# Kernel optimization log

Hardware: AMD Instinct MI355X
Metric: run time of the kernel (lower is better)

## Reference

```python
import jax, jax.numpy as jnp
import numpy as np

B, T, H, M = 8, 2048, 1024, 256


def setup_inputs() -> dict:
    key = jax.random.key(0)
    ks = jax.random.split(key, 8)
    hidden_states = jax.random.normal(ks[0], (B, T, H), jnp.float32)
    incoming_signal = jax.random.normal(ks[1], (B, T, H), jnp.float32)
    top_down = jax.random.normal(ks[2], (B, T, H), jnp.float32)
    basis = jax.random.normal(ks[3], (B, H, M), jnp.float32) / np.float32(np.sqrt(H))
    # coupling L = G^-1; near identity for a near-orthonormal basis
    coupling = jnp.tile(jnp.eye(M, dtype=jnp.float32), (B, 1, 1)) + 0.01 * jax.random.normal(ks[4], (B, M, M), jnp.float32)
    W_rec = jax.random.normal(ks[5], (2 * M, H), jnp.float32) / np.float32(np.sqrt(2 * M))
    tape0_re = 0.1 * jax.random.normal(ks[6], (B, M), jnp.float32)
    tape0_im = 0.1 * jax.random.normal(ks[7], (B, M), jnp.float32)
    # raw metaparams: sigmoid(gamma_raw)=0.9, softplus(beta_raw)=0.05 (init values in source)
    gamma_raw = jnp.float32(np.log(0.9 / 0.1))
    beta_raw = jnp.float32(np.log(np.expm1(0.05)))
    return dict(hidden_states=hidden_states, incoming_signal=incoming_signal, top_down=top_down,
                basis=basis, coupling=coupling, W_rec=W_rec, tape0_re=tape0_re, tape0_im=tape0_im,
                bottom_up_gain=jnp.float32(1.0), top_down_gain=jnp.float32(1.0), self_rec_gain=jnp.float32(1.0),
                gamma_raw=gamma_raw, beta_raw=beta_raw)


def reference(hidden_states, incoming_signal, top_down, basis, coupling, W_rec,
              tape0_re, tape0_im, bottom_up_gain, top_down_gain, self_rec_gain,
              gamma_raw, beta_raw):
    gamma = jax.nn.sigmoid(gamma_raw)      # transient decay
    beta = jax.nn.softplus(beta_raw)       # binding scale
    # gated combination of external + bottom-up + top-down signals
    combined = hidden_states + bottom_up_gain * incoming_signal + top_down_gain * top_down  # [B,T,H]
    # delayed self-recurrence: project real/imag tape features back into hidden space
    tape_feat = jnp.concatenate([tape0_re, tape0_im], axis=-1)          # [B,2M]
    combined = combined + self_rec_gain * (tape_feat @ W_rec)[:, None, :]
    # coupled reception (vectorized over tokens): w = E^T v ; alpha = L w
    w = jnp.einsum('btd,bdm->btm', combined, basis)                     # [B,T,M]
    alpha = jnp.einsum('btm,bmn->btn', w, coupling)                     # [B,T,M]
    # recurrent tape update (binding write + transient decay), c = alpha * s
    def step(carry, a_t):
        s_re, s_im = carry
        s_re = gamma * s_re + beta * a_t
        s_im = gamma * s_im
        return (s_re, s_im), a_t * s_re
    (_, _), c_re = jax.lax.scan(step, (tape0_re, tape0_im), jnp.swapaxes(alpha, 0, 1))
    c_re = jnp.swapaxes(c_re, 0, 1)                                     # [B,T,M]
    # readout through the basis
    y = jnp.einsum('btm,bdm->btd', c_re, basis)                         # [B,T,H]
    return y
```

## Files before the change

### kernel.cpp

```cpp
#include <hip/hip_runtime.h>
#include <hip/hip_bf16.h>

#define B_  8
#define T_  2048
#define H_  1024
#define M_  256

typedef __bf16 bf16x8 __attribute__((ext_vector_type(8)));
typedef float  f32x4  __attribute__((ext_vector_type(4)));
typedef unsigned short us4 __attribute__((ext_vector_type(4)));
typedef unsigned short us8 __attribute__((ext_vector_type(8)));

__device__ inline unsigned short f2bf(float f) {
    unsigned int u = __builtin_bit_cast(unsigned int, f);
    return (unsigned short)((u + 0x7FFFu + ((u >> 16) & 1u)) >> 16);
}
__device__ inline float bf2f(unsigned short u) {
    unsigned int x = ((unsigned int)u) << 16;
    return __builtin_bit_cast(float, x);
}

__global__ void k_bias(const float* __restrict__ W, const float* __restrict__ re,
                       const float* __restrict__ im, const float* __restrict__ g_srg,
                       float* __restrict__ bias)
{
    int b = blockIdx.x;
    int h0 = blockIdx.y * 64;
    int lane = threadIdx.x & 63, w = threadIdx.x >> 6;
    int h = h0 + lane;
    float acc = 0.f;
    #pragma unroll 4
    for (int m = w * 64; m < w * 64 + 64; ++m) {
        float rv = re[b * M_ + m], iv = im[b * M_ + m];
        acc += rv * W[(size_t)m * H_ + h] + iv * W[(size_t)(M_ + m) * H_ + h];
    }
    __shared__ float sh[4][64];
    sh[w][lane] = acc;
    __syncthreads();
    if (w == 0)
        bias[b * H_ + h] = g_srg[0] * (sh[0][lane] + sh[1][lane] + sh[2][lane] + sh[3][lane]);
}

__global__ void k_cast(const float* __restrict__ basis, unsigned short* __restrict__ basisB)
{
    size_t i = ((size_t)blockIdx.x * 256 + threadIdx.x) * 8;
    float4 a = *(const float4*)&basis[i];
    float4 b = *(const float4*)&basis[i + 4];
    us8 o = { f2bf(a.x), f2bf(a.y), f2bf(a.z), f2bf(a.w),
              f2bf(b.x), f2bf(b.y), f2bf(b.z), f2bf(b.w) };
    *(us8*)&basisB[i] = o;
}

__global__ void k_cplT(const float* __restrict__ cpl, unsigned short* __restrict__ cplT)
{
    int b = blockIdx.z, r0 = blockIdx.x * 64, c0 = blockIdx.y * 64;
    __shared__ float t[64][65];
    int tid = threadIdx.x;
    #pragma unroll
    for (int i = 0; i < 4; ++i) {
        int u = tid + i * 256;
        int r = u >> 4, c4 = (u & 15) * 4;
        float4 v = *(const float4*)&cpl[((size_t)(b * M_ + r0 + r)) * M_ + c0 + c4];
        t[r][c4] = v.x; t[r][c4 + 1] = v.y; t[r][c4 + 2] = v.z; t[r][c4 + 3] = v.w;
    }
    __syncthreads();
    #pragma unroll
    for (int i = 0; i < 4; ++i) {
        int u = tid + i * 256;
        int m = u >> 4, r4 = (u & 15) * 4;
        us4 o = { f2bf(t[r4][m]), f2bf(t[r4 + 1][m]), f2bf(t[r4 + 2][m]), f2bf(t[r4 + 3][m]) };
        *(us4*)&cplT[((size_t)(b * M_ + c0 + m)) * M_ + r0 + r4] = o;
    }
}

__global__ __launch_bounds__(256) void k_b2(const unsigned short* __restrict__ cplT,
                                            const unsigned short* __restrict__ basisB,
                                            unsigned short* __restrict__ b2T)
{
    const int b = blockIdx.z;
    const int n0 = blockIdx.x * 64;
    const int h0 = blockIdx.y * 128;
    const int tid = threadIdx.x;
    const int lane = tid & 63, w = tid >> 6;

    __shared__ __align__(16) unsigned short As[64][72];
    __shared__ __align__(16) unsigned short Bs[128][72];

    const unsigned short* Ab = cplT + (size_t)(b * M_ + n0) * M_;
    const unsigned short* Bb = basisB + (size_t)(b * H_ + h0) * M_;

    f32x4 acc[4][2];
    #pragma unroll
    for (int i = 0; i < 4; ++i) { acc[i][0] = (f32x4){0,0,0,0}; acc[i][1] = (f32x4){0,0,0,0}; }

    const int rsel = lane & 15;
    const int kgrp = (lane >> 4) * 8;

    for (int k0 = 0; k0 < M_; k0 += 64) {
        #pragma unroll
        for (int i = 0; i < 2; ++i) {
            int u = tid + i * 256;
            int r = u >> 3, c8 = (u & 7) * 8;
            *(us8*)&As[r][c8] = *(const us8*)&Ab[(size_t)r * M_ + k0 + c8];
        }
        #pragma unroll
        for (int i = 0; i < 4; ++i) {
            int u = tid + i * 256;
            int r = u >> 3, c8 = (u & 7) * 8;
            *(us8*)&Bs[r][c8] = *(const us8*)&Bb[(size_t)r * M_ + k0 + c8];
        }
        __syncthreads();
        #pragma unroll
        for (int kk = 0; kk < 2; ++kk) {
            const int kb = kk * 32 + kgrp;
            bf16x8 af[4], bfr[2];
            #pragma unroll
            for (int mi = 0; mi < 4; ++mi) af[mi] = *(const bf16x8*)&As[mi * 16 + rsel][kb];
            #pragma unroll
            for (int ni = 0; ni < 2; ++ni) bfr[ni] = *(const bf16x8*)&Bs[w * 32 + ni * 16 + rsel][kb];
            #pragma unroll
            for (int mi = 0; mi < 4; ++mi)
                #pragma unroll
                for (int ni = 0; ni < 2; ++ni)
                    acc[mi][ni] = __builtin_amdgcn_mfma_f32_16x16x32_bf16(af[mi], bfr[ni], acc[mi][ni], 0, 0, 0);
        }
        __syncthreads();
    }

    unsigned short* ob = b2T + (size_t)(b * M_ + n0) * H_ + h0;
    const int rbase = (lane >> 4) * 4;
    #pragma unroll
    for (int mi = 0; mi < 4; ++mi)
        #pragma unroll
        for (int ni = 0; ni < 2; ++ni)
            #pragma unroll
            for (int r = 0; r < 4; ++r)
                ob[(size_t)(mi * 16 + rbase + r) * H_ + w * 32 + ni * 16 + rsel] = f2bf(acc[mi][ni][r]);
}

__global__ __launch_bounds__(1024) void k_alpha(
    const float* __restrict__ hs, const float* __restrict__ inc, const float* __restrict__ tdn,
    const unsigned short* __restrict__ b2T, const float* __restrict__ bias,
    const float* __restrict__ g_bu, const float* __restrict__ g_td,
    unsigned short* __restrict__ alpha16)
{
    const int b = blockIdx.y;
    const int t0 = blockIdx.x * 64;
    const int tid = threadIdx.x;
    const int lane = tid & 63, w = tid >> 6;
    const float bug = g_bu[0], tdg = g_td[0];

    __shared__ __align__(16) unsigned short As[64][72];
    __shared__ __align__(16) unsigned short Bs[256][72];

    const float* hsb = hs  + (size_t)(b * T_ + t0) * H_;
    const float* inb = inc + (size_t)(b * T_ + t0) * H_;
    const float* tdb = tdn + (size_t)(b * T_ + t0) * H_;
    const float* bib = bias + (size_t)b * H_;
    const unsigned short* Bb = b2T + (size_t)b * M_ * H_;

    f32x4 acc[4];
    #pragma unroll
    for (int i = 0; i < 4; ++i) acc[i] = (f32x4){0.f, 0.f, 0.f, 0.f};

    const int rsel = lane & 15;
    const int kgrp = (lane >> 4) * 8;

    for (int k0 = 0; k0 < H_; k0 += 64) {
        {
            int r = tid >> 4, c4 = (tid & 15) * 4;
            size_t g = (size_t)r * H_ + k0 + c4;
            float4 a = *(const float4*)(hsb + g);
            float4 e = *(const float4*)(inb + g);
            float4 d = *(const float4*)(tdb + g);
            float4 bi = *(const float4*)(bib + k0 + c4);
            us4 o = { f2bf(a.x + bug * e.x + tdg * d.x + bi.x),
                      f2bf(a.y + bug * e.y + tdg * d.y + bi.y),
                      f2bf(a.z + bug * e.z + tdg * d.z + bi.z),
                      f2bf(a.w + bug * e.w + tdg * d.w + bi.w) };
            *(us4*)&As[r][c4] = o;
        }
        #pragma unroll
        for (int i = 0; i < 2; ++i) {
            int u = tid + i * 1024;
            int m = u >> 3, c8 = (u & 7) * 8;
            *(us8*)&Bs[m][c8] = *(const us8*)&Bb[(size_t)m * H_ + k0 + c8];
        }
        __syncthreads();
        #pragma unroll
        for (int kk = 0; kk < 2; ++kk) {
            const int kb = kk * 32 + kgrp;
            bf16x8 af[4], bfr;
            #pragma unroll
            for (int mi = 0; mi < 4; ++mi) af[mi] = *(const bf16x8*)&As[mi * 16 + rsel][kb];
            bfr = *(const bf16x8*)&Bs[w * 16 + rsel][kb];
            #pragma unroll
            for (int mi = 0; mi < 4; ++mi)
                acc[mi] = __builtin_amdgcn_mfma_f32_16x16x32_bf16(af[mi], bfr, acc[mi], 0, 0, 0);
        }
        __syncthreads();
    }

    unsigned short* ab = alpha16 + (size_t)(b * T_ + t0) * M_;
    const int rbase = (lane >> 4) * 4;
    #pragma unroll
    for (int mi = 0; mi < 4; ++mi)
        #pragma unroll
        for (int r = 0; r < 4; ++r)
            ab[(size_t)(mi * 16 + rbase + r) * M_ + w * 16 + rsel] = f2bf(acc[mi][r]);
}

__global__ void k_scan(const unsigned short* __restrict__ alpha16, const float* __restrict__ tape_re,
                       const float* __restrict__ g_gr, const float* __restrict__ g_br,
                       unsigned short* __restrict__ cbuf)
{
    int b = blockIdx.y, chunk = blockIdx.x;
    int m = threadIdx.x;
    float graw = g_gr[0], braw = g_br[0];
    float gamma = 1.f / (1.f + __expf(-graw));
    float beta  = log1pf(__expf(braw));
    int t0 = chunk * 64;
    int th = (t0 >= 96) ? (t0 - 96) : 0;
    float s = tape_re[b * M_ + m];
    if (th > 0) s *= __powf(gamma, (float)th);
    const unsigned short* ab = alpha16 + (size_t)b * T_ * M_ + m;
    unsigned short* cb = cbuf + (size_t)b * T_ * M_ + m;
    for (int t = th; t < t0 + 64; ++t) {
        float a = bf2f(ab[(size_t)t * M_]);
        s = gamma * s + beta * a;
        if (t >= t0) cb[(size_t)t * M_] = f2bf(a * s);
    }
}

__global__ __launch_bounds__(256) void k_y(const unsigned short* __restrict__ cbuf,
                                           const unsigned short* __restrict__ basisB,
                                           float* __restrict__ out)
{
    const int b = blockIdx.z;
    const int t0 = blockIdx.x * 128;
    const int h0 = blockIdx.y * 128;
    const int tid = threadIdx.x;
    const int lane = tid & 63, w = tid >> 6;
    const int wm = w >> 1, wn = w & 1;

    __shared__ __align__(16) unsigned short As[128][72];
    __shared__ __align__(16) unsigned short Bs[128][72];

    const unsigned short* cb = cbuf + (size_t)(b * T_ + t0) * M_;
    const unsigned short* bb = basisB + (size_t)(b * H_ + h0) * M_;

    f32x4 acc[4][4];
    #pragma unroll
    for (int i = 0; i < 4; ++i)
        #pragma unroll
        for (int j = 0; j < 4; ++j)
            acc[i][j] = (f32x4){0.f, 0.f, 0.f, 0.f};

    const int rsel = lane & 15;
    const int kgrp = (lane >> 4) * 8;

    for (int k0 = 0; k0 < M_; k0 += 64) {
        #pragma unroll
        for (int i = 0; i < 4; ++i) {
            int u = tid + i * 256;
            int r = u >> 3, c8 = (u & 7) * 8;
            *(us8*)&As[r][c8] = *(const us8*)&cb[(size_t)r * M_ + k0 + c8];
        }
        #pragma unroll
        for (int i = 0; i < 4; ++i) {
            int u = tid + i * 256;
            int r = u >> 3, c8 = (u & 7) * 8;
            *(us8*)&Bs[r][c8] = *(const us8*)&bb[(size_t)r * M_ + k0 + c8];
        }
        __syncthreads();
        #pragma unroll
        for (int kk = 0; kk < 2; ++kk) {
            const int kb = kk * 32 + kgrp;
            bf16x8 af[4], bfr[4];
            #pragma unroll
            for (int mi = 0; mi < 4; ++mi) af[mi] = *(const bf16x8*)&As[wm * 64 + mi * 16 + rsel][kb];
            #pragma unroll
            for (int ni = 0; ni < 4; ++ni) bfr[ni] = *(const bf16x8*)&Bs[wn * 64 + ni * 16 + rsel][kb];
            #pragma unroll
            for (int mi = 0; mi < 4; ++mi)
                #pragma unroll
                for (int ni = 0; ni < 4; ++ni)
                    acc[mi][ni] = __builtin_amdgcn_mfma_f32_16x16x32_bf16(af[mi], bfr[ni], acc[mi][ni], 0, 0, 0);
        }
        __syncthreads();
    }

    float* ob = out + (size_t)(b * T_ + t0) * H_ + h0;
    const int rbase = (lane >> 4) * 4;
    #pragma unroll
    for (int mi = 0; mi < 4; ++mi)
        #pragma unroll
        for (int ni = 0; ni < 4; ++ni)
            #pragma unroll
            for (int r = 0; r < 4; ++r)
                ob[(size_t)(wm * 64 + mi * 16 + rbase + r) * H_ + wn * 64 + ni * 16 + rsel] = acc[mi][ni][r];
}

extern "C" void kernel_launch(void* const* d_in, const int* in_sizes, int n_in,
                              void* d_out, int out_size, void* d_ws, size_t ws_size,
                              hipStream_t stream)
{
    const float* hs   = (const float*)d_in[0];
    const float* inc  = (const float*)d_in[1];
    const float* tdn  = (const float*)d_in[2];
    const float* basis= (const float*)d_in[3];
    const float* cpl  = (const float*)d_in[4];
    const float* W    = (const float*)d_in[5];
    const float* t_re = (const float*)d_in[6];
    const float* t_im = (const float*)d_in[7];
    const float* g_bu = (const float*)d_in[8];
    const float* g_td = (const float*)d_in[9];
    const float* g_sr = (const float*)d_in[10];
    const float* g_gr = (const float*)d_in[11];
    const float* g_br = (const float*)d_in[12];
    float* out = (float*)d_out;

    char* ws = (char*)d_ws;
    float*          bias   = (float*)(ws);
    unsigned short* basisB = (unsigned short*)(ws + (1u << 16));
    unsigned short* cplT   = (unsigned short*)(ws + (1u << 16) + (4u << 20));
    unsigned short* b2T    = (unsigned short*)(ws + (1u << 16) + (5u << 20));
    unsigned short* alpha16= (unsigned short*)(ws + (1u << 16) + (9u << 20));
    unsigned short* cbuf   = (unsigned short*)(ws + (1u << 16) + (17u << 20));

    k_bias <<<dim3(B_, H_ / 64),            dim3(256),  0, stream>>>(W, t_re, t_im, g_sr, bias);
    k_cast <<<dim3((B_ * H_ * M_) / (256*8)), dim3(256), 0, stream>>>(basis, basisB);
    k_cplT <<<dim3(M_ / 64, M_ / 64, B_),   dim3(256),  0, stream>>>(cpl, cplT);
    k_b2   <<<dim3(M_ / 64, H_ / 128, B_),  dim3(256),  0, stream>>>(cplT, basisB, b2T);
    k_alpha<<<dim3(T_ / 64, B_),            dim3(1024), 0, stream>>>(hs, inc, tdn, b2T, bias, g_bu, g_td, alpha16);
    k_scan <<<dim3(T_ / 64, B_),            dim3(256),  0, stream>>>(alpha16, t_re, g_gr, g_br, cbuf);
    k_y    <<<dim3(T_ / 128, H_ / 128, B_), dim3(256),  0, stream>>>(cbuf, basisB, out);
}
```

Measured before the change: 152.6 us.

## Merge prep kernels and register-prefetch the alpha GEMM with smaller tiles

Result: faster. 149.5 us (-2.0%).

```diff
diff --git a/kernel.cpp b/kernel.cpp
--- a/kernel.cpp
+++ b/kernel.cpp
@@ -20,56 +20,57 @@
     return __builtin_bit_cast(float, x);
 }
 
-__global__ void k_bias(const float* __restrict__ W, const float* __restrict__ re,
+__global__ void k_prep(const float* __restrict__ basis, const float* __restrict__ cpl,
+                       const float* __restrict__ W, const float* __restrict__ re,
                        const float* __restrict__ im, const float* __restrict__ g_srg,
+                       unsigned short* __restrict__ basisB, unsigned short* __restrict__ cplT,
                        float* __restrict__ bias)
 {
-    int b = blockIdx.x;
-    int h0 = blockIdx.y * 64;
-    int lane = threadIdx.x & 63, w = threadIdx.x >> 6;
-    int h = h0 + lane;
-    float acc = 0.f;
-    #pragma unroll 4
-    for (int m = w * 64; m < w * 64 + 64; ++m) {
-        float rv = re[b * M_ + m], iv = im[b * M_ + m];
-        acc += rv * W[(size_t)m * H_ + h] + iv * W[(size_t)(M_ + m) * H_ + h];
-    }
-    __shared__ float sh[4][64];
-    sh[w][lane] = acc;
-    __syncthreads();
-    if (w == 0)
-        bias[b * H_ + h] = g_srg[0] * (sh[0][lane] + sh[1][lane] + sh[2][lane] + sh[3][lane]);
-}
-
-__global__ void k_cast(const float* __restrict__ basis, unsigned short* __restrict__ basisB)
-{
-    size_t i = ((size_t)blockIdx.x * 256 + threadIdx.x) * 8;
-    float4 a = *(const float4*)&basis[i];
-    float4 b = *(const float4*)&basis[i + 4];
-    us8 o = { f2bf(a.x), f2bf(a.y), f2bf(a.z), f2bf(a.w),
-              f2bf(b.x), f2bf(b.y), f2bf(b.z), f2bf(b.w) };
-    *(us8*)&basisB[i] = o;
-}
-
-__global__ void k_cplT(const float* __restrict__ cpl, unsigned short* __restrict__ cplT)
-{
-    int b = blockIdx.z, r0 = blockIdx.x * 64, c0 = blockIdx.y * 64;
-    __shared__ float t[64][65];
+    int blk = blockIdx.x;
     int tid = threadIdx.x;
-    #pragma unroll
-    for (int i = 0; i < 4; ++i) {
-        int u = tid + i * 256;
-        int r = u >> 4, c4 = (u & 15) * 4;
-        float4 v = *(const float4*)&cpl[((size_t)(b * M_ + r0 + r)) * M_ + c0 + c4];
-        t[r][c4] = v.x; t[r][c4 + 1] = v.y; t[r][c4 + 2] = v.z; t[r][c4 + 3] = v.w;
-    }
-    __syncthreads();
-    #pragma unroll
-    for (int i = 0; i < 4; ++i) {
-        int u = tid + i * 256;
-        int m = u >> 4, r4 = (u & 15) * 4;
-        us4 o = { f2bf(t[r4][m]), f2bf(t[r4 + 1][m]), f2bf(t[r4 + 2][m]), f2bf(t[r4 + 3][m]) };
-        *(us4*)&cplT[((size_t)(b * M_ + c0 + m)) * M_ + r0 + r4] = o;
+    if (blk < 1024) {
+        size_t i = ((size_t)blk * 256 + tid) * 8;
+        float4 a = *(const float4*)&basis[i];
+        float4 b = *(const float4*)&basis[i + 4];
+        us8 o = { f2bf(a.x), f2bf(a.y), f2bf(a.z), f2bf(a.w),
+                  f2bf(b.x), f2bf(b.y), f2bf(b.z), f2bf(b.w) };
+        *(us8*)&basisB[i] = o;
+    } else if (blk < 1152) {
+        int idx = blk - 1024;
+        int x = idx & 3, y = (idx >> 2) & 3, b = idx >> 4;
+        int r0 = x * 64, c0 = y * 64;
+        __shared__ float t[64][65];
+        #pragma unroll
+        for (int i = 0; i < 4; ++i) {
+            int u = tid + i * 256;
+            int r = u >> 4, c4 = (u & 15) * 4;
+            float4 v = *(const float4*)&cpl[((size_t)(b * M_ + r0 + r)) * M_ + c0 + c4];
+            t[r][c4] = v.x; t[r][c4 + 1] = v.y; t[r][c4 + 2] = v.z; t[r][c4 + 3] = v.w;
+        }
+        __syncthreads();
+        #pragma unroll
+        for (int i = 0; i < 4; ++i) {
+            int u = tid + i * 256;
+            int m = u >> 4, r4 = (u & 15) * 4;
+            us4 o = { f2bf(t[r4][m]), f2bf(t[r4 + 1][m]), f2bf(t[r4 + 2][m]), f2bf(t[r4 + 3][m]) };
+            *(us4*)&cplT[((size_t)(b * M_ + c0 + m)) * M_ + r0 + r4] = o;
+        }
+    } else {
+        int idx = blk - 1152;
+        int b = idx & 7, h0 = (idx >> 3) * 64;
+        int lane = tid & 63, w = tid >> 6;
+        int h = h0 + lane;
+        float acc = 0.f;
+        #pragma unroll 4
+        for (int m = w * 64; m < w * 64 + 64; ++m) {
+            float rv = re[b * M_ + m], iv = im[b * M_ + m];
+            acc += rv * W[(size_t)m * H_ + h] + iv * W[(size_t)(M_ + m) * H_ + h];
+        }
+        __shared__ float sh[4][64];
+        sh[w][lane] = acc;
+        __syncthreads();
+        if (w == 0)
+            bias[b * H_ + h] = g_srg[0] * (sh[0][lane] + sh[1][lane] + sh[2][lane] + sh[3][lane]);
     }
 }
 
@@ -138,19 +139,19 @@
                 ob[(size_t)(mi * 16 + rbase + r) * H_ + w * 32 + ni * 16 + rsel] = f2bf(acc[mi][ni][r]);
 }
 
-__global__ __launch_bounds__(1024) void k_alpha(
+__global__ __launch_bounds__(512) void k_alpha(
     const float* __restrict__ hs, const float* __restrict__ inc, const float* __restrict__ tdn,
     const unsigned short* __restrict__ b2T, const float* __restrict__ bias,
     const float* __restrict__ g_bu, const float* __restrict__ g_td,
     unsigned short* __restrict__ alpha16)
 {
     const int b = blockIdx.y;
-    const int t0 = blockIdx.x * 64;
+    const int t0 = blockIdx.x * 32;
     const int tid = threadIdx.x;
     const int lane = tid & 63, w = tid >> 6;
     const float bug = g_bu[0], tdg = g_td[0];
 
-    __shared__ __align__(16) unsigned short As[64][72];
+    __shared__ __align__(16) unsigned short As[32][72];
     __shared__ __align__(16) unsigned short Bs[256][72];
 
     const float* hsb = hs  + (size_t)(b * T_ + t0) * H_;
@@ -159,55 +160,85 @@
     const float* bib = bias + (size_t)b * H_;
     const unsigned short* Bb = b2T + (size_t)b * M_ * H_;
 
-    f32x4 acc[4];
-    #pragma unroll
-    for (int i = 0; i < 4; ++i) acc[i] = (f32x4){0.f, 0.f, 0.f, 0.f};
+    const int ar  = tid >> 4;
+    const int ac4 = (tid & 15) * 4;
+    const int br0 = tid >> 3;
+    const int bc8 = (tid & 7) * 8;
+
+    f32x4 acc[2][2];
+    acc[0][0] = (f32x4){0,0,0,0}; acc[0][1] = (f32x4){0,0,0,0};
+    acc[1][0] = (f32x4){0,0,0,0}; acc[1][1] = (f32x4){0,0,0,0};
 
     const int rsel = lane & 15;
     const int kgrp = (lane >> 4) * 8;
 
-    for (int k0 = 0; k0 < H_; k0 += 64) {
-        {
-            int r = tid >> 4, c4 = (tid & 15) * 4;
-            size_t g = (size_t)r * H_ + k0 + c4;
-            float4 a = *(const float4*)(hsb + g);
-            float4 e = *(const float4*)(inb + g);
-            float4 d = *(const float4*)(tdb + g);
-            float4 bi = *(const float4*)(bib + k0 + c4);
-            us4 o = { f2bf(a.x + bug * e.x + tdg * d.x + bi.x),
-                      f2bf(a.y + bug * e.y + tdg * d.y + bi.y),
-                      f2bf(a.z + bug * e.z + tdg * d.z + bi.z),
-                      f2bf(a.w + bug * e.w + tdg * d.w + bi.w) };
-            *(us4*)&As[r][c4] = o;
-        }
-        #pragma unroll
-        for (int i = 0; i < 2; ++i) {
-            int u = tid + i * 1024;
-            int m = u >> 3, c8 = (u & 7) * 8;
-            *(us8*)&Bs[m][c8] = *(const us8*)&Bb[(size_t)m * H_ + k0 + c8];
-        }
-        __syncthreads();
-        #pragma unroll
-        for (int kk = 0; kk < 2; ++kk) {
-            const int kb = kk * 32 + kgrp;
-            bf16x8 af[4], bfr;
-            #pragma unroll
-            for (int mi = 0; mi < 4; ++mi) af[mi] = *(const bf16x8*)&As[mi * 16 + rsel][kb];
-            bfr = *(const bf16x8*)&Bs[w * 16 + rsel][kb];
-            #pragma unroll
-            for (int mi = 0; mi < 4; ++mi)
-                acc[mi] = __builtin_amdgcn_mfma_f32_16x16x32_bf16(af[mi], bfr, acc[mi], 0, 0, 0);
-        }
-        __syncthreads();
-    }
+    float4 pa, pe, pd, pbv;
+    us8 pB0, pB1, pB2, pB3;
+
+    #define LOAD_TILE(K0) do {                                                  \
+        size_t g = (size_t)ar * H_ + (K0) + ac4;                                \
+        pa  = *(const float4*)(hsb + g);                                        \
+        pe  = *(const float4*)(inb + g);                                        \
+        pd  = *(const float4*)(tdb + g);                                        \
+        pbv = *(const float4*)(bib + (K0) + ac4);                               \
+        pB0 = *(const us8*)&Bb[(size_t)(br0      ) * H_ + (K0) + bc8];          \
+        pB1 = *(const us8*)&Bb[(size_t)(br0 +  64) * H_ + (K0) + bc8];          \
+        pB2 = *(const us8*)&Bb[(size_t)(br0 + 128) * H_ + (K0) + bc8];          \
+        pB3 = *(const us8*)&Bb[(size_t)(br0 + 192) * H_ + (K0) + bc8];          \
+    } while (0)
+
+    #define STORE_TILE() do {                                                   \
+        us4 o = { f2bf(pa.x + bug * pe.x + tdg * pd.x + pbv.x),                 \
+                  f2bf(pa.y + bug * pe.y + tdg * pd.y + pbv.y),                 \
+                  f2bf(pa.z + bug * pe.z + tdg * pd.z + pbv.z),                 \
+                  f2bf(pa.w + bug * pe.w + tdg * pd.w + pbv.w) };               \
+        *(us4*)&As[ar][ac4] = o;                                                \
+        *(us8*)&Bs[br0      ][bc8] = pB0;                                       \
+        *(us8*)&Bs[br0 +  64][bc8] = pB1;                                       \
+        *(us8*)&Bs[br0 + 128][bc8] = pB2;                                       \
+        *(us8*)&Bs[br0 + 192][bc8] = pB3;                                       \
+    } while (0)
+
+    #define COMPUTE_TILE() do {                                                 \
+        _Pragma("unroll")                                                       \
+        for (int kk = 0; kk < 2; ++kk) {                                        \
+            const int kb = kk * 32 + kgrp;                                      \
+            bf16x8 af0 = *(const bf16x8*)&As[rsel][kb];                         \
+            bf16x8 af1 = *(const bf16x8*)&As[16 + rsel][kb];                    \
+            bf16x8 bf0 = *(const bf16x8*)&Bs[w * 32 + rsel][kb];                \
+            bf16x8 bf1 = *(const bf16x8*)&Bs[w * 32 + 16 + rsel][kb];           \
+            acc[0][0] = __builtin_amdgcn_mfma_f32_16x16x32_bf16(af0, bf0, acc[0][0], 0, 0, 0); \
+            acc[0][1] = __builtin_amdgcn_mfma_f32_16x16x32_bf16(af0, bf1, acc[0][1], 0, 0, 0); \
+            acc[1][0] = __builtin_amdgcn_mfma_f32_16x16x32_bf16(af1, bf0, acc[1][0], 0, 0, 0); \
+            acc[1][1] = __builtin_amdgcn_mfma_f32_16x16x32_bf16(af1, bf1, acc[1][1], 0, 0, 0); \
+        }                                                                       \
+    } while (0)
+
+    LOAD_TILE(0);
+    STORE_TILE();
+    __syncthreads();
+    for (int k0 = 64; k0 < H_; k0 += 64) {
+        LOAD_TILE(k0);
+        COMPUTE_TILE();
+        __syncthreads();
+        STORE_TILE();
+        __syncthreads();
+    }
+    COMPUTE_TILE();
+
+    #undef LOAD_TILE
+    #undef STORE_TILE
+    #undef COMPUTE_TILE
 
     unsigned short* ab = alpha16 + (size_t)(b * T_ + t0) * M_;
     const int rbase = (lane >> 4) * 4;
     #pragma unroll
-    for (int mi = 0; mi < 4; ++mi)
-        #pragma unroll
-        for (int r = 0; r < 4; ++r)
-            ab[(size_t)(mi * 16 + rbase + r) * M_ + w * 16 + rsel] = f2bf(acc[mi][r]);
+    for (int mi = 0; mi < 2; ++mi)
+        #pragma unroll
+        for (int ni = 0; ni < 2; ++ni)
+            #pragma unroll
+            for (int r = 0; r < 4; ++r)
+                ab[(size_t)(mi * 16 + rbase + r) * M_ + w * 32 + ni * 16 + rsel] = f2bf(acc[mi][ni][r]);
 }
 
 __global__ void k_scan(const unsigned short* __restrict__ alpha16, const float* __restrict__ tape_re,
@@ -328,11 +359,9 @@
     unsigned short* alpha16= (unsigned short*)(ws + (1u << 16) + (9u << 20));
     unsigned short* cbuf   = (unsigned short*)(ws + (1u << 16) + (17u << 20));
 
-    k_bias <<<dim3(B_, H_ / 64),            dim3(256),  0, stream>>>(W, t_re, t_im, g_sr, bias);
-    k_cast <<<dim3((B_ * H_ * M_) / (256*8)), dim3(256), 0, stream>>>(basis, basisB);
-    k_cplT <<<dim3(M_ / 64, M_ / 64, B_),   dim3(256),  0, stream>>>(cpl, cplT);
+    k_prep <<<dim3(1280),                   dim3(256),  0, stream>>>(basis, cpl, W, t_re, t_im, g_sr, basisB, cplT, bias);
     k_b2   <<<dim3(M_ / 64, H_ / 128, B_),  dim3(256),  0, stream>>>(cplT, basisB, b2T);
-    k_alpha<<<dim3(T_ / 64, B_),            dim3(1024), 0, stream>>>(hs, inc, tdn, b2T, bias, g_bu, g_td, alpha16);
+    k_alpha<<<dim3(T_ / 32, B_),            dim3(512),  0, stream>>>(hs, inc, tdn, b2T, bias, g_bu, g_td, alpha16);
     k_scan <<<dim3(T_ / 64, B_),            dim3(256),  0, stream>>>(alpha16, t_re, g_gr, g_br, cbuf);
     k_y    <<<dim3(T_ / 128, H_ / 128, B_), dim3(256),  0, stream>>>(cbuf, basisB, out);
 }
```

## Fuse prep kernels and rework alpha GEMM as register-direct split-K

Applied to the files above, without the earlier changes.

Measured after the change: 216.7 us. 42.0% more time.

```diff
diff --git a/kernel.cpp b/kernel.cpp
--- a/kernel.cpp
+++ b/kernel.cpp
@@ -20,56 +20,57 @@
     return __builtin_bit_cast(float, x);
 }
 
-__global__ void k_bias(const float* __restrict__ W, const float* __restrict__ re,
+__global__ void k_prep(const float* __restrict__ basis, const float* __restrict__ cpl,
+                       const float* __restrict__ W, const float* __restrict__ re,
                        const float* __restrict__ im, const float* __restrict__ g_srg,
+                       unsigned short* __restrict__ basisB, unsigned short* __restrict__ cplT,
                        float* __restrict__ bias)
 {
-    int b = blockIdx.x;
-    int h0 = blockIdx.y * 64;
-    int lane = threadIdx.x & 63, w = threadIdx.x >> 6;
-    int h = h0 + lane;
-    float acc = 0.f;
-    #pragma unroll 4
-    for (int m = w * 64; m < w * 64 + 64; ++m) {
-        float rv = re[b * M_ + m], iv = im[b * M_ + m];
-        acc += rv * W[(size_t)m * H_ + h] + iv * W[(size_t)(M_ + m) * H_ + h];
-    }
-    __shared__ float sh[4][64];
-    sh[w][lane] = acc;
-    __syncthreads();
-    if (w == 0)
-        bias[b * H_ + h] = g_srg[0] * (sh[0][lane] + sh[1][lane] + sh[2][lane] + sh[3][lane]);
-}
-
-__global__ void k_cast(const float* __restrict__ basis, unsigned short* __restrict__ basisB)
-{
-    size_t i = ((size_t)blockIdx.x * 256 + threadIdx.x) * 8;
-    float4 a = *(const float4*)&basis[i];
-    float4 b = *(const float4*)&basis[i + 4];
-    us8 o = { f2bf(a.x), f2bf(a.y), f2bf(a.z), f2bf(a.w),
-              f2bf(b.x), f2bf(b.y), f2bf(b.z), f2bf(b.w) };
-    *(us8*)&basisB[i] = o;
-}
-
-__global__ void k_cplT(const float* __restrict__ cpl, unsigned short* __restrict__ cplT)
-{
-    int b = blockIdx.z, r0 = blockIdx.x * 64, c0 = blockIdx.y * 64;
-    __shared__ float t[64][65];
+    int blk = blockIdx.x;
     int tid = threadIdx.x;
-    #pragma unroll
-    for (int i = 0; i < 4; ++i) {
-        int u = tid + i * 256;
-        int r = u >> 4, c4 = (u & 15) * 4;
-        float4 v = *(const float4*)&cpl[((size_t)(b * M_ + r0 + r)) * M_ + c0 + c4];
-        t[r][c4] = v.x; t[r][c4 + 1] = v.y; t[r][c4 + 2] = v.z; t[r][c4 + 3] = v.w;
-    }
-    __syncthreads();
-    #pragma unroll
-    for (int i = 0; i < 4; ++i) {
-        int u = tid + i * 256;
-        int m = u >> 4, r4 = (u & 15) * 4;
-        us4 o = { f2bf(t[r4][m]), f2bf(t[r4 + 1][m]), f2bf(t[r4 + 2][m]), f2bf(t[r4 + 3][m]) };
-        *(us4*)&cplT[((size_t)(b * M_ + c0 + m)) * M_ + r0 + r4] = o;
+    if (blk < 1024) {
+        size_t i = ((size_t)blk * 256 + tid) * 8;
+        float4 a = *(const float4*)&basis[i];
+        float4 b = *(const float4*)&basis[i + 4];
+        us8 o = { f2bf(a.x), f2bf(a.y), f2bf(a.z), f2bf(a.w),
+                  f2bf(b.x), f2bf(b.y), f2bf(b.z), f2bf(b.w) };
+        *(us8*)&basisB[i] = o;
+    } else if (blk < 1152) {
+        int idx = blk - 1024;
+        int x = idx & 3, y = (idx >> 2) & 3, b = idx >> 4;
+        int r0 = x * 64, c0 = y * 64;
+        __shared__ float t[64][65];
+        #pragma unroll
+        for (int i = 0; i < 4; ++i) {
+            int u = tid + i * 256;
+            int r = u >> 4, c4 = (u & 15) * 4;
+            float4 v = *(const float4*)&cpl[((size_t)(b * M_ + r0 + r)) * M_ + c0 + c4];
+            t[r][c4] = v.x; t[r][c4 + 1] = v.y; t[r][c4 + 2] = v.z; t[r][c4 + 3] = v.w;
+        }
+        __syncthreads();
+        #pragma unroll
+        for (int i = 0; i < 4; ++i) {
+            int u = tid + i * 256;
+            int m = u >> 4, r4 = (u & 15) * 4;
+            us4 o = { f2bf(t[r4][m]), f2bf(t[r4 + 1][m]), f2bf(t[r4 + 2][m]), f2bf(t[r4 + 3][m]) };
+            *(us4*)&cplT[((size_t)(b * M_ + c0 + m)) * M_ + r0 + r4] = o;
+        }
+    } else {
+        int idx = blk - 1152;
+        int b = idx & 7, h0 = (idx >> 3) * 64;
+        int lane = tid & 63, w = tid >> 6;
+        int h = h0 + lane;
+        float acc = 0.f;
+        #pragma unroll 4
+        for (int m = w * 64; m < w * 64 + 64; ++m) {
+            float rv = re[b * M_ + m], iv = im[b * M_ + m];
+            acc += rv * W[(size_t)m * H_ + h] + iv * W[(size_t)(M_ + m) * H_ + h];
+        }
+        __shared__ float sh[4][64];
+        sh[w][lane] = acc;
+        __syncthreads();
+        if (w == 0)
+            bias[b * H_ + h] = g_srg[0] * (sh[0][lane] + sh[1][lane] + sh[2][lane] + sh[3][lane]);
     }
 }
 
@@ -138,79 +139,70 @@
                 ob[(size_t)(mi * 16 + rbase + r) * H_ + w * 32 + ni * 16 + rsel] = f2bf(acc[mi][ni][r]);
 }
 
-__global__ __launch_bounds__(1024) void k_alpha(
+__global__ __launch_bounds__(256, 4) void k_alpha(
     const float* __restrict__ hs, const float* __restrict__ inc, const float* __restrict__ tdn,
     const unsigned short* __restrict__ b2T, const float* __restrict__ bias,
     const float* __restrict__ g_bu, const float* __restrict__ g_td,
-    unsigned short* __restrict__ alpha16)
-{
-    const int b = blockIdx.y;
-    const int t0 = blockIdx.x * 64;
+    unsigned short* __restrict__ pal)
+{
+    const int flat = blockIdx.x;
+    const int b = flat & 7;
+    const int t0 = (flat >> 3) * 16;
     const int tid = threadIdx.x;
-    const int lane = tid & 63, w = tid >> 6;
+    const int lane = tid & 63, wid = tid >> 6;
+    const int mh = (wid & 1) * 128;
+    const int kh = (wid >> 1) * 512;
+    const int rsel = lane & 15;
+    const int kgo = (lane >> 4) * 8;
     const float bug = g_bu[0], tdg = g_td[0];
 
-    __shared__ __align__(16) unsigned short As[64][72];
-    __shared__ __align__(16) unsigned short Bs[256][72];
-
-    const float* hsb = hs  + (size_t)(b * T_ + t0) * H_;
-    const float* inb = inc + (size_t)(b * T_ + t0) * H_;
-    const float* tdb = tdn + (size_t)(b * T_ + t0) * H_;
-    const float* bib = bias + (size_t)b * H_;
-    const unsigned short* Bb = b2T + (size_t)b * M_ * H_;
-
-    f32x4 acc[4];
-    #pragma unroll
-    for (int i = 0; i < 4; ++i) acc[i] = (f32x4){0.f, 0.f, 0.f, 0.f};
-
-    const int rsel = lane & 15;
-    const int kgrp = (lane >> 4) * 8;
-
-    for (int k0 = 0; k0 < H_; k0 += 64) {
-        {
-            int r = tid >> 4, c4 = (tid & 15) * 4;
-            size_t g = (size_t)r * H_ + k0 + c4;
-            float4 a = *(const float4*)(hsb + g);
-            float4 e = *(const float4*)(inb + g);
-            float4 d = *(const float4*)(tdb + g);
-            float4 bi = *(const float4*)(bib + k0 + c4);
-            us4 o = { f2bf(a.x + bug * e.x + tdg * d.x + bi.x),
-                      f2bf(a.y + bug * e.y + tdg * d.y + bi.y),
-                      f2bf(a.z + bug * e.z + tdg * d.z + bi.z),
-                      f2bf(a.w + bug * e.w + tdg * d.w + bi.w) };
-            *(us4*)&As[r][c4] = o;
-        }
-        #pragma unroll
-        for (int i = 0; i < 2; ++i) {
-            int u = tid + i * 1024;
-            int m = u >> 3, c8 = (u & 7) * 8;
-            *(us8*)&Bs[m][c8] = *(const us8*)&Bb[(size_t)m * H_ + k0 + c8];
-        }
-        __syncthreads();
-        #pragma unroll
-        for (int kk = 0; kk < 2; ++kk) {
-            const int kb = kk * 32 + kgrp;
-            bf16x8 af[4], bfr;
-            #pragma unroll
-            for (int mi = 0; mi < 4; ++mi) af[mi] = *(const bf16x8*)&As[mi * 16 + rsel][kb];
-            bfr = *(const bf16x8*)&Bs[w * 16 + rsel][kb];
-            #pragma unroll
-            for (int mi = 0; mi < 4; ++mi)
-                acc[mi] = __builtin_amdgcn_mfma_f32_16x16x32_bf16(af[mi], bfr, acc[mi], 0, 0, 0);
-        }
-        __syncthreads();
-    }
-
-    unsigned short* ab = alpha16 + (size_t)(b * T_ + t0) * M_;
+    const size_t rb = ((size_t)(b * T_) + t0 + rsel) * H_ + kh + kgo;
+    const float* hs0 = hs + rb;
+    const float* in0 = inc + rb;
+    const float* td0 = tdn + rb;
+    const float* bib = bias + b * H_ + kh + kgo;
+    const unsigned short* Bb = b2T + ((size_t)(b * M_) + mh + rsel) * H_ + kh + kgo;
+
+    f32x4 acc[8];
+    #pragma unroll
+    for (int i = 0; i < 8; ++i) acc[i] = (f32x4){0.f, 0.f, 0.f, 0.f};
+
+    #pragma unroll 2
+    for (int kb = 0; kb < 512; kb += 32) {
+        f32x4 bi0 = *(const f32x4*)(bib + kb);
+        f32x4 bi1 = *(const f32x4*)(bib + kb + 4);
+        f32x4 a0 = *(const f32x4*)(hs0 + kb), a1 = *(const f32x4*)(hs0 + kb + 4);
+        f32x4 e0 = *(const f32x4*)(in0 + kb), e1 = *(const f32x4*)(in0 + kb + 4);
+        f32x4 d0 = *(const f32x4*)(td0 + kb), d1 = *(const f32x4*)(td0 + kb + 4);
+
+        f32x4 c0 = a0 + bug * e0 + tdg * d0 + bi0;
+        f32x4 c1 = a1 + bug * e1 + tdg * d1 + bi1;
+
+        bf16x8 af;
+        #pragma unroll
+        for (int j = 0; j < 4; ++j) {
+            af[j]     = (__bf16)c0[j];
+            af[j + 4] = (__bf16)c1[j];
+        }
+
+        #pragma unroll
+        for (int ni = 0; ni < 8; ++ni) {
+            bf16x8 bv = *(const bf16x8*)(Bb + (size_t)ni * (16 * H_) + kb);
+            acc[ni] = __builtin_amdgcn_mfma_f32_16x16x32_bf16(af, bv, acc[ni], 0, 0, 0);
+        }
+    }
+
+    unsigned short* ab = pal + (size_t)(wid >> 1) * ((size_t)B_ * T_ * M_)
+                       + ((size_t)(b * T_) + t0) * M_ + mh;
     const int rbase = (lane >> 4) * 4;
     #pragma unroll
-    for (int mi = 0; mi < 4; ++mi)
+    for (int ni = 0; ni < 8; ++ni)
         #pragma unroll
         for (int r = 0; r < 4; ++r)
-            ab[(size_t)(mi * 16 + rbase + r) * M_ + w * 16 + rsel] = f2bf(acc[mi][r]);
-}
-
-__global__ void k_scan(const unsigned short* __restrict__ alpha16, const float* __restrict__ tape_re,
+            ab[(size_t)(rbase + r) * M_ + ni * 16 + rsel] = f2bf(acc[ni][r]);
+}
+
+__global__ void k_scan(const unsigned short* __restrict__ pal, const float* __restrict__ tape_re,
                        const float* __restrict__ g_gr, const float* __restrict__ g_br,
                        unsigned short* __restrict__ cbuf)
 {
@@ -223,10 +215,13 @@
     int th = (t0 >= 96) ? (t0 - 96) : 0;
     float s = tape_re[b * M_ + m];
     if (th > 0) s *= __powf(gamma, (float)th);
-    const unsigned short* ab = alpha16 + (size_t)b * T_ * M_ + m;
+    const size_t PH = (size_t)B_ * T_ * M_;
+    const unsigned short* p0 = pal + (size_t)b * T_ * M_ + m;
+    const unsigned short* p1 = p0 + PH;
     unsigned short* cb = cbuf + (size_t)b * T_ * M_ + m;
+    #pragma unroll 4
     for (int t = th; t < t0 + 64; ++t) {
-        float a = bf2f(ab[(size_t)t * M_]);
+        float a = bf2f(p0[(size_t)t * M_]) + bf2f(p1[(size_t)t * M_]);
         s = gamma * s + beta * a;
         if (t >= t0) cb[(size_t)t * M_] = f2bf(a * s);
     }
@@ -325,14 +320,12 @@
     unsigned short* basisB = (unsigned short*)(ws + (1u << 16));
     unsigned short* cplT   = (unsigned short*)(ws + (1u << 16) + (4u << 20));
     unsigned short* b2T    = (unsigned short*)(ws + (1u << 16) + (5u << 20));
-    unsigned short* alpha16= (unsigned short*)(ws + (1u << 16) + (9u << 20));
-    unsigned short* cbuf   = (unsigned short*)(ws + (1u << 16) + (17u << 20));
-
-    k_bias <<<dim3(B_, H_ / 64),            dim3(256),  0, stream>>>(W, t_re, t_im, g_sr, bias);
-    k_cast <<<dim3((B_ * H_ * M_) / (256*8)), dim3(256), 0, stream>>>(basis, basisB);
-    k_cplT <<<dim3(M_ / 64, M_ / 64, B_),   dim3(256),  0, stream>>>(cpl, cplT);
-    k_b2   <<<dim3(M_ / 64, H_ / 128, B_),  dim3(256),  0, stream>>>(cplT, basisB, b2T);
-    k_alpha<<<dim3(T_ / 64, B_),            dim3(1024), 0, stream>>>(hs, inc, tdn, b2T, bias, g_bu, g_td, alpha16);
-    k_scan <<<dim3(T_ / 64, B_),            dim3(256),  0, stream>>>(alpha16, t_re, g_gr, g_br, cbuf);
-    k_y    <<<dim3(T_ / 128, H_ / 128, B_), dim3(256),  0, stream>>>(cbuf, basisB, out);
-}
+    unsigned short* pal    = (unsigned short*)(ws + (1u << 16) + (9u << 20));
+    unsigned short* cbuf   = (unsigned short*)(ws + (1u << 16) + (25u << 20));
+
+    k_prep <<<dim3(1280),                   dim3(256), 0, stream>>>(basis, cpl, W, t_re, t_im, g_sr, basisB, cplT, bias);
+    k_b2   <<<dim3(M_ / 64, H_ / 128, B_),  dim3(256), 0, stream>>>(cplT, basisB, b2T);
+    k_alpha<<<dim3(1024),                   dim3(256), 0, stream>>>(hs, inc, tdn, b2T, bias, g_bu, g_td, pal);
+    k_scan <<<dim3(T_ / 64, B_),            dim3(256), 0, stream>>>(pal, t_re, g_gr, g_br, cbuf);
+    k_y    <<<dim3(T_ / 128, H_ / 128, B_), dim3(256), 0, stream>>>(cbuf, basisB, out);
+}
```
